# Optimization experiments

Measured on AMD Instinct MI355X. Metric: run time of the kernel, lower is better.

The kernel has to match this reference:

```python
import jax, jax.numpy as jnp
import numpy as np

E = 512      # embed_dim
H = 8        # num_heads
D = E // H   # head_dim = 64
R = 32       # rot_dims (partial rotary)
THETA = 10000.0


def _rope(x):
    # x: [B, H, S, D]; rotate first R dims (interleaved pairs, lucidrains-style)
    S = x.shape[-2]
    inv_freq = THETA ** (-jnp.arange(0, R, 2, dtype=jnp.float32) / R)  # [R/2]
    ang = jnp.arange(S, dtype=jnp.float32)[:, None] * inv_freq          # [S, R/2]
    c, s = jnp.cos(ang), jnp.sin(ang)
    xr, xp = x[..., :R], x[..., R:]
    x1, x2 = xr[..., 0::2], xr[..., 1::2]
    rot = jnp.stack([x1 * c - x2 * s, x1 * s + x2 * c], axis=-1).reshape(xr.shape)
    return jnp.concatenate([rot, xp], axis=-1)


def setup_inputs() -> dict:
    key = jax.random.key(0)
    k1, k2, k3, k4 = jax.random.split(key, 4)
    B, S = 4, 2048
    x = jax.random.normal(k1, (B, S, E), dtype=jnp.float32)
    input_mask = jax.random.randint(k2, (B, S), 0, 2).astype(bool)
    W_in = jax.random.normal(k3, (3 * E, E), dtype=jnp.float32) / np.sqrt(E).astype(np.float32)
    W_out = jax.random.normal(k4, (E, E), dtype=jnp.float32) / np.sqrt(E).astype(np.float32)
    return {"x": x, "input_mask": input_mask, "W_in": W_in, "W_out": W_out}


def reference(x, input_mask, W_in, W_out):
    B, S, _ = x.shape
    # fused QKV projection (Linear, no bias): x @ W_in.T -> [B,S,3E]
    qkv = (x @ W_in.T).reshape(B, S, 3, H, D).transpose(2, 0, 3, 1, 4)  # [3,B,H,S,D]
    q, k, v = qkv[0], qkv[1], qkv[2]
    q = _rope(q)
    k = _rope(k)
    # mask: causal AND (both tokens valid OR diagonal)
    causal = jnp.tril(jnp.ones((S, S), dtype=bool))
    inv = ~input_mask                                  # [B,S]
    cross = inv[:, None, :] | inv[:, :, None]          # [B,S,S]
    square = (~cross) | jnp.eye(S, dtype=bool)         # diagonal forced True
    full = causal[None, :, :] & square                 # [B,S,S]
    scores = jnp.einsum('bhsd,bhtd->bhst', q, k) / np.float32(np.sqrt(D))
    scores = jnp.where(full[:, None, :, :], scores, -jnp.inf)
    probs = jax.nn.softmax(scores, axis=-1)
    attn = jnp.einsum('bhst,bhtd->bhsd', probs, v)
    attn = attn.transpose(0, 2, 1, 3).reshape(B, S, E)
    return attn @ W_out.T
```

## Files before the change

kernel.cpp:

```cpp
#include <hip/hip_runtime.h>
#include <math.h>

#define B_ 4
#define S_ 2048
#define E_ 512
#define H_ 8
#define D_ 64

typedef short bf16x8 __attribute__((ext_vector_type(8)));
typedef float f32x4 __attribute__((ext_vector_type(4)));

__device__ inline short f2bf(float f) {
  union { float f; unsigned u; } v; v.f = f;
  unsigned r = v.u + 0x7FFF + ((v.u >> 16) & 1);
  return (short)(r >> 16);
}
__device__ inline short f2bf_fast(float f) {
  union { float f; unsigned u; } v; v.f = f;
  return (short)((v.u + 0x8000u) >> 16);
}
__device__ inline float bf2f(short s) {
  union { unsigned u; float f; } v; v.u = ((unsigned)(unsigned short)s) << 16;
  return v.f;
}

__global__ __launch_bounds__(256) void cvt_bf16(const float* __restrict__ src,
                                                short* __restrict__ dst, int n4) {
  int i = blockIdx.x * 256 + threadIdx.x;
  if (i < n4) {
    float4 f = ((const float4*)src)[i];
    short4 o;
    o.x = f2bf(f.x); o.y = f2bf(f.y); o.z = f2bf(f.z); o.w = f2bf(f.w);
    ((short4*)dst)[i] = o;
  }
}

__global__ __launch_bounds__(256) void gemm_qkv_mfma(
    const short* __restrict__ Xb,
    const short* __restrict__ Wb,
    short* __restrict__ qb, short* __restrict__ kb, short* __restrict__ vbT) {
  __shared__ __align__(16) short As[128][40];
  __shared__ __align__(16) short Bs[128][40];
  const int tid = threadIdx.x;
  const int w = tid >> 6, lane = tid & 63;
  const int l15 = lane & 15, quad = lane >> 4;
  const int wm = w & 1, wn = w >> 1;
  const int m0 = blockIdx.x * 128;
  const int n0 = blockIdx.y * 128;
  f32x4 acc[4][4];
  for (int mt = 0; mt < 4; ++mt)
    for (int nt = 0; nt < 4; ++nt) acc[mt][nt] = (f32x4){0.f, 0.f, 0.f, 0.f};

  for (int k0 = 0; k0 < E_; k0 += 32) {
    __syncthreads();
    for (int l = 0; l < 2; ++l) {
      int c = tid + 256 * l;
      int row = c >> 2, k8 = (c & 3) * 8;
      *(bf16x8*)&As[row][k8] = *(const bf16x8*)&Xb[(size_t)(m0 + row) * E_ + k0 + k8];
      *(bf16x8*)&Bs[row][k8] = *(const bf16x8*)&Wb[(size_t)(n0 + row) * E_ + k0 + k8];
    }
    __syncthreads();
    bf16x8 a[4], bfr[4];
    for (int mt = 0; mt < 4; ++mt)
      a[mt] = *(const bf16x8*)&As[wm * 64 + mt * 16 + l15][quad * 8];
    for (int nt = 0; nt < 4; ++nt)
      bfr[nt] = *(const bf16x8*)&Bs[wn * 64 + nt * 16 + l15][quad * 8];
    for (int mt = 0; mt < 4; ++mt)
      for (int nt = 0; nt < 4; ++nt)
        acc[mt][nt] = __builtin_amdgcn_mfma_f32_16x16x32_bf16(a[mt], bfr[nt], acc[mt][nt], 0, 0, 0);
  }
  const int t3 = n0 >> 9;
  for (int nt = 0; nt < 4; ++nt) {
    const int n = n0 + wn * 64 + nt * 16 + l15;
    const int h = (n >> 6) & 7;
    const int d = n & 63;
    const bool dorope = (t3 < 2) && (d < 32);
    const float sgn = (d & 1) ? 1.f : -1.f;
    const float fr = dorope ? powf(10000.f, -(float)(2 * (d >> 1)) * (1.f / 32.f)) : 0.f;
    for (int mt = 0; mt < 4; ++mt) {
      for (int i = 0; i < 4; ++i) {
        const int m = m0 + wm * 64 + mt * 16 + quad * 4 + i;
        const int b = m >> 11, s = m & (S_ - 1);
        float val = acc[mt][nt][i];
        float pv = __shfl_xor(val, 1, 64);
        float outv = val;
        if (dorope) {
          float ang = (float)s * fr;
          float sn, cs;
          sincosf(ang, &sn, &cs);
          outv = val * cs + pv * sgn * sn;
        }
        if (t3 == 2)
          vbT[((size_t)(b * 8 + h) * D_ + d) * S_ + s] = f2bf(outv);
        else {
          short* dst = (t3 == 0) ? qb : kb;
          dst[(((size_t)(b * 8 + h)) * S_ + s) * D_ + d] = f2bf(outv);
        }
      }
    }
  }
}

__global__ __launch_bounds__(256) void gemm_out_mfma(
    const short* __restrict__ Ab, const short* __restrict__ Wb,
    float* __restrict__ out) {
  __shared__ __align__(16) short As[128][40];
  __shared__ __align__(16) short Bs[128][40];
  const int tid = threadIdx.x;
  const int w = tid >> 6, lane = tid & 63;
  const int l15 = lane & 15, quad = lane >> 4;
  const int wm = w & 1, wn = w >> 1;
  const int m0 = blockIdx.x * 128;
  const int n0 = blockIdx.y * 128;
  f32x4 acc[4][4];
  for (int mt = 0; mt < 4; ++mt)
    for (int nt = 0; nt < 4; ++nt) acc[mt][nt] = (f32x4){0.f, 0.f, 0.f, 0.f};

  for (int k0 = 0; k0 < E_; k0 += 32) {
    __syncthreads();
    for (int l = 0; l < 2; ++l) {
      int c = tid + 256 * l;
      int row = c >> 2, k8 = (c & 3) * 8;
      *(bf16x8*)&As[row][k8] = *(const bf16x8*)&Ab[(size_t)(m0 + row) * E_ + k0 + k8];
      *(bf16x8*)&Bs[row][k8] = *(const bf16x8*)&Wb[(size_t)(n0 + row) * E_ + k0 + k8];
    }
    __syncthreads();
    bf16x8 a[4], bfr[4];
    for (int mt = 0; mt < 4; ++mt)
      a[mt] = *(const bf16x8*)&As[wm * 64 + mt * 16 + l15][quad * 8];
    for (int nt = 0; nt < 4; ++nt)
      bfr[nt] = *(const bf16x8*)&Bs[wn * 64 + nt * 16 + l15][quad * 8];
    for (int mt = 0; mt < 4; ++mt)
      for (int nt = 0; nt < 4; ++nt)
        acc[mt][nt] = __builtin_amdgcn_mfma_f32_16x16x32_bf16(a[mt], bfr[nt], acc[mt][nt], 0, 0, 0);
  }
  for (int mt = 0; mt < 4; ++mt)
    for (int nt = 0; nt < 4; ++nt) {
      const int n = n0 + wn * 64 + nt * 16 + l15;
      for (int i = 0; i < 4; ++i) {
        const int m = m0 + wm * 64 + mt * 16 + quad * 4 + i;
        out[(size_t)m * E_ + n] = acc[mt][nt][i];
      }
    }
}

__global__ __launch_bounds__(256) void flash_mfma(
    const short* __restrict__ qb, const short* __restrict__ kb,
    const short* __restrict__ vbT, const int* __restrict__ maskp,
    short* __restrict__ pb0, short* __restrict__ pb1,
    float* __restrict__ lb0, float* __restrict__ lb1,
    short* __restrict__ ob) {
  __shared__ __align__(16) short Ks[64][72];
  __shared__ __align__(16) short VT[64][72];
  __shared__ __align__(16) short Pl[4][16][72];
  __shared__ float kbias[64];
  const int tid = threadIdx.x;
  const int w = tid >> 6, lane = tid & 63;
  const int l15 = lane & 15, quad = lane >> 4;
  const int bid = blockIdx.x;
  const int u = bid & 7, v = bid >> 3;
  const int bh = (u << 2) | (v & 3);
  const int w2 = v >> 2;
  const int pair = w2 & 15;
  const int kh = w2 >> 4;
  const int b = bh >> 3, hd = bh & 7;
  const short* qbase = qb + (size_t)bh * S_ * D_;
  const short* kbase = kb + (size_t)bh * S_ * D_;
  const short* vtb   = vbT + (size_t)bh * D_ * S_;
  short* PB = kh ? pb1 : pb0;
  float* LB = kh ? lb1 : lb0;
  const float c2 = 0.1803368801f;
  bf16x8 ones;
  for (int j = 0; j < 8; ++j) ones[j] = (short)0x3F80;

  for (int seg = 0; seg < 2; ++seg) {
    const int qt = (seg == 0) ? pair : 31 - pair;
    const int r0 = qt * 64;
    const int mid = (qt + 2) >> 1;
    const int lo = kh ? mid : 0;
    const int hi = kh ? (qt + 1) : mid;
    bf16x8 aq[2];
    {
      const short* qrow = qbase + (size_t)(r0 + 16 * w + l15) * D_;
      aq[0] = *(const bf16x8*)&qrow[quad * 8];
      aq[1] = *(const bf16x8*)&qrow[32 + quad * 8];
    }
    f32x4 o[4], lsum;
    for (int no = 0; no < 4; ++no) o[no] = (f32x4){0.f, 0.f, 0.f, 0.f};
    lsum = (f32x4){0.f, 0.f, 0.f, 0.f};

    for (int kt = lo; kt < hi; ++kt) {
      const int t0 = kt * 64;
      __syncthreads();
      for (int l = 0; l < 2; ++l) {
        int idx = tid + 256 * l;
        int row = idx >> 3, ch = (idx & 7) * 8;
        *(bf16x8*)&Ks[row][ch] = *(const bf16x8*)(kbase + (size_t)(t0 + row) * D_ + ch);
        *(bf16x8*)&VT[row][ch] = *(const bf16x8*)(vtb + (size_t)row * S_ + t0 + ch);
      }
      if (tid < 64)
        kbias[tid] = maskp[b * S_ + t0 + tid] ? -23.08312f : -1.0e38f;
      __syncthreads();
      f32x4 sfr[4];
      for (int nb = 0; nb < 4; ++nb) sfr[nb] = (f32x4){0.f, 0.f, 0.f, 0.f};
      for (int nb = 0; nb < 4; ++nb)
        for (int ks = 0; ks < 2; ++ks) {
          bf16x8 bk = *(const bf16x8*)&Ks[l15 + 16 * nb][32 * ks + quad * 8];
          sfr[nb] = __builtin_amdgcn_mfma_f32_16x16x32_bf16(aq[ks], bk, sfr[nb], 0, 0, 0);
        }
      if (kt < qt) {
        for (int nb = 0; nb < 4; ++nb) {
          const float bb = kbias[l15 + 16 * nb];
          for (int i = 0; i < 4; ++i)
            Pl[w][quad * 4 + i][l15 + 16 * nb] = f2bf_fast(exp2f(sfr[nb][i] * c2 + bb));
        }
      } else {
        for (int nb = 0; nb < 4; ++nb) {
          const int tg = l15 + 16 * nb;
          const float bb = kbias[l15 + 16 * nb];
          for (int i = 0; i < 4; ++i) {
            const float bbi = (tg > 16 * w + quad * 4 + i) ? -1.0e38f : bb;
            Pl[w][quad * 4 + i][l15 + 16 * nb] = f2bf_fast(exp2f(sfr[nb][i] * c2 + bbi));
          }
        }
      }
      asm volatile("s_waitcnt lgkmcnt(0)" ::: "memory");
      bf16x8 ap0 = *(const bf16x8*)&Pl[w][l15][quad * 8];
      bf16x8 ap1 = *(const bf16x8*)&Pl[w][l15][32 + quad * 8];
      for (int no = 0; no < 4; ++no) {
        bf16x8 bv0 = *(const bf16x8*)&VT[16 * no + l15][quad * 8];
        bf16x8 bv1 = *(const bf16x8*)&VT[16 * no + l15][32 + quad * 8];
        o[no] = __builtin_amdgcn_mfma_f32_16x16x32_bf16(ap0, bv0, o[no], 0, 0, 0);
        o[no] = __builtin_amdgcn_mfma_f32_16x16x32_bf16(ap1, bv1, o[no], 0, 0, 0);
      }
      lsum = __builtin_amdgcn_mfma_f32_16x16x32_bf16(ap0, ones, lsum, 0, 0, 0);
      lsum = __builtin_amdgcn_mfma_f32_16x16x32_bf16(ap1, ones, lsum, 0, 0, 0);
    }
    for (int i = 0; i < 4; ++i) {
      const int s = r0 + 16 * w + quad * 4 + i;
      const int qm = maskp[b * S_ + s];
      const size_t row = (size_t)(b * S_ + s) * E_ + hd * D_;
      if (kh == 0 && !qm) {
        for (int no = 0; no < 4; ++no) {
          const int d = l15 + 16 * no;
          ob[row + d] = vtb[(size_t)d * S_ + s];
        }
      }
      for (int no = 0; no < 4; ++no)
        PB[row + l15 + 16 * no] = f2bf(o[no][i]);
      if (l15 == 0)
        LB[bh * S_ + s] = lsum[i];
    }
  }
}

__global__ __launch_bounds__(256) void merge_kernel(
    const short* __restrict__ pb0, const short* __restrict__ pb1,
    const float* __restrict__ lb0, const float* __restrict__ lb1,
    const int* __restrict__ maskp, short* __restrict__ ob) {
  int idx = blockIdx.x * 256 + threadIdx.x;
  int m = idx >> 6, e = (idx & 63) * 8;
  if (!maskp[m]) return;
  int b = m >> 11, s = m & (S_ - 1);
  int bh = b * 8 + (e >> 6);
  float l = lb0[bh * S_ + s] + lb1[bh * S_ + s];
  float inv = 1.f / l;
  bf16x8 p0 = *(const bf16x8*)&pb0[(size_t)m * E_ + e];
  bf16x8 p1 = *(const bf16x8*)&pb1[(size_t)m * E_ + e];
  bf16x8 r;
  for (int j = 0; j < 8; ++j)
    r[j] = f2bf((bf2f(p0[j]) + bf2f(p1[j])) * inv);
  *(bf16x8*)&ob[(size_t)m * E_ + e] = r;
}

extern "C" void kernel_launch(void* const* d_in, const int* in_sizes, int n_in,
                              void* d_out, int out_size, void* d_ws, size_t ws_size,
                              hipStream_t stream) {
  const float* x    = (const float*)d_in[0];
  const int*   mask = (const int*)d_in[1];
  const float* Win  = (const float*)d_in[2];
  const float* Wout = (const float*)d_in[3];
  float* out = (float*)d_out;

  short* Xb    = (short*)d_ws;
  short* Winb  = Xb + 8192 * 512;
  short* Woutb = Winb + 1536 * 512;
  short* qb    = Woutb + 512 * 512;
  short* kb    = qb + 32 * 2048 * 64;
  short* vbT   = kb + 32 * 2048 * 64;
  short* ob    = vbT + 32 * 2048 * 64;
  short* pb0   = ob + 8192 * 512;
  short* pb1   = pb0 + 8192 * 512;
  float* lb0   = (float*)(pb1 + 8192 * 512);
  float* lb1   = lb0 + 32 * 2048;

  cvt_bf16<<<4096, 256, 0, stream>>>(x, Xb, 8192 * 512 / 4);
  cvt_bf16<<<768, 256, 0, stream>>>(Win, Winb, 1536 * 512 / 4);
  cvt_bf16<<<256, 256, 0, stream>>>(Wout, Woutb, 512 * 512 / 4);
  gemm_qkv_mfma<<<dim3(64, 12), 256, 0, stream>>>(Xb, Winb, qb, kb, vbT);
  flash_mfma<<<1024, 256, 0, stream>>>(qb, kb, vbT, mask, pb0, pb1, lb0, lb1, ob);
  merge_kernel<<<2048, 256, 0, stream>>>(pb0, pb1, lb0, lb1, mask, ob);
  gemm_out_mfma<<<dim3(64, 4), 256, 0, stream>>>(ob, Woutb, out);
}
```

Before: 178.3 us.

## Double-buffer LDS in projection GEMMs and merge conversion launches

Both projection GEMMs now use two LDS buffers: the global loads for the next K-slice are issued into registers before the MFMAs on the current slice and stored to the other buffer afterwards, leaving one barrier per iteration instead of two. The three fp32-to-bf16 conversion kernels are merged into one launch that picks its source by block index. The RoPE epilogue switches sincosf to the faster, lower-precision __sincosf intrinsic. The aim is to hide global load latency and cut launch overhead, at the cost of doubled LDS use and more live registers.

```diff
diff --git a/kernel.cpp b/kernel.cpp
--- a/kernel.cpp
+++ b/kernel.cpp
@@ -24,50 +24,78 @@
   return v.f;
 }
 
-__global__ __launch_bounds__(256) void cvt_bf16(const float* __restrict__ src,
-                                                short* __restrict__ dst, int n4) {
-  int i = blockIdx.x * 256 + threadIdx.x;
-  if (i < n4) {
-    float4 f = ((const float4*)src)[i];
-    short4 o;
-    o.x = f2bf(f.x); o.y = f2bf(f.y); o.z = f2bf(f.z); o.w = f2bf(f.w);
-    ((short4*)dst)[i] = o;
-  }
+__global__ __launch_bounds__(256) void cvt_all(
+    const float* __restrict__ x, const float* __restrict__ win,
+    const float* __restrict__ wout, short* __restrict__ xb,
+    short* __restrict__ winb, short* __restrict__ woutb) {
+  int bid = blockIdx.x;
+  const float* src; short* dst; int i;
+  if (bid < 4096)      { src = x;    dst = xb;    i = bid * 256 + threadIdx.x; }
+  else if (bid < 4864) { src = win;  dst = winb;  i = (bid - 4096) * 256 + threadIdx.x; }
+  else                 { src = wout; dst = woutb; i = (bid - 4864) * 256 + threadIdx.x; }
+  float4 f = ((const float4*)src)[i];
+  short4 o;
+  o.x = f2bf(f.x); o.y = f2bf(f.y); o.z = f2bf(f.z); o.w = f2bf(f.w);
+  ((short4*)dst)[i] = o;
 }
 
 __global__ __launch_bounds__(256) void gemm_qkv_mfma(
     const short* __restrict__ Xb,
     const short* __restrict__ Wb,
     short* __restrict__ qb, short* __restrict__ kb, short* __restrict__ vbT) {
-  __shared__ __align__(16) short As[128][40];
-  __shared__ __align__(16) short Bs[128][40];
+  __shared__ __align__(16) short As[2][128][40];
+  __shared__ __align__(16) short Bs[2][128][40];
   const int tid = threadIdx.x;
   const int w = tid >> 6, lane = tid & 63;
   const int l15 = lane & 15, quad = lane >> 4;
   const int wm = w & 1, wn = w >> 1;
   const int m0 = blockIdx.x * 128;
   const int n0 = blockIdx.y * 128;
+  const int r0s = tid >> 2,        k80 = (tid & 3) * 8;
+  const int r1s = (tid + 256) >> 2, k81 = ((tid + 256) & 3) * 8;
+  const short* gA0 = &Xb[(size_t)(m0 + r0s) * E_ + k80];
+  const short* gA1 = &Xb[(size_t)(m0 + r1s) * E_ + k81];
+  const short* gB0 = &Wb[(size_t)(n0 + r0s) * E_ + k80];
+  const short* gB1 = &Wb[(size_t)(n0 + r1s) * E_ + k81];
   f32x4 acc[4][4];
   for (int mt = 0; mt < 4; ++mt)
     for (int nt = 0; nt < 4; ++nt) acc[mt][nt] = (f32x4){0.f, 0.f, 0.f, 0.f};
 
-  for (int k0 = 0; k0 < E_; k0 += 32) {
-    __syncthreads();
-    for (int l = 0; l < 2; ++l) {
-      int c = tid + 256 * l;
-      int row = c >> 2, k8 = (c & 3) * 8;
-      *(bf16x8*)&As[row][k8] = *(const bf16x8*)&Xb[(size_t)(m0 + row) * E_ + k0 + k8];
-      *(bf16x8*)&Bs[row][k8] = *(const bf16x8*)&Wb[(size_t)(n0 + row) * E_ + k0 + k8];
-    }
-    __syncthreads();
+  bf16x8 ra0 = *(const bf16x8*)gA0;
+  bf16x8 ra1 = *(const bf16x8*)gA1;
+  bf16x8 rb0 = *(const bf16x8*)gB0;
+  bf16x8 rb1 = *(const bf16x8*)gB1;
+  *(bf16x8*)&As[0][r0s][k80] = ra0;
+  *(bf16x8*)&As[0][r1s][k81] = ra1;
+  *(bf16x8*)&Bs[0][r0s][k80] = rb0;
+  *(bf16x8*)&Bs[0][r1s][k81] = rb1;
+  __syncthreads();
+
+  for (int kt = 0; kt < 16; ++kt) {
+    const int cur = kt & 1;
+    if (kt < 15) {
+      const int k0 = (kt + 1) * 32;
+      ra0 = *(const bf16x8*)(gA0 + k0);
+      ra1 = *(const bf16x8*)(gA1 + k0);
+      rb0 = *(const bf16x8*)(gB0 + k0);
+      rb1 = *(const bf16x8*)(gB1 + k0);
+    }
     bf16x8 a[4], bfr[4];
     for (int mt = 0; mt < 4; ++mt)
-      a[mt] = *(const bf16x8*)&As[wm * 64 + mt * 16 + l15][quad * 8];
+      a[mt] = *(const bf16x8*)&As[cur][wm * 64 + mt * 16 + l15][quad * 8];
     for (int nt = 0; nt < 4; ++nt)
-      bfr[nt] = *(const bf16x8*)&Bs[wn * 64 + nt * 16 + l15][quad * 8];
+      bfr[nt] = *(const bf16x8*)&Bs[cur][wn * 64 + nt * 16 + l15][quad * 8];
     for (int mt = 0; mt < 4; ++mt)
       for (int nt = 0; nt < 4; ++nt)
         acc[mt][nt] = __builtin_amdgcn_mfma_f32_16x16x32_bf16(a[mt], bfr[nt], acc[mt][nt], 0, 0, 0);
+    if (kt < 15) {
+      const int nxt = cur ^ 1;
+      *(bf16x8*)&As[nxt][r0s][k80] = ra0;
+      *(bf16x8*)&As[nxt][r1s][k81] = ra1;
+      *(bf16x8*)&Bs[nxt][r0s][k80] = rb0;
+      *(bf16x8*)&Bs[nxt][r1s][k81] = rb1;
+    }
+    __syncthreads();
   }
   const int t3 = n0 >> 9;
   for (int nt = 0; nt < 4; ++nt) {
@@ -85,9 +113,8 @@
         float pv = __shfl_xor(val, 1, 64);
         float outv = val;
         if (dorope) {
-          float ang = (float)s * fr;
           float sn, cs;
-          sincosf(ang, &sn, &cs);
+          __sincosf((float)s * fr, &sn, &cs);
           outv = val * cs + pv * sgn * sn;
         }
         if (t3 == 2)
@@ -104,35 +131,59 @@
 __global__ __launch_bounds__(256) void gemm_out_mfma(
     const short* __restrict__ Ab, const short* __restrict__ Wb,
     float* __restrict__ out) {
-  __shared__ __align__(16) short As[128][40];
-  __shared__ __align__(16) short Bs[128][40];
+  __shared__ __align__(16) short As[2][128][40];
+  __shared__ __align__(16) short Bs[2][128][40];
   const int tid = threadIdx.x;
   const int w = tid >> 6, lane = tid & 63;
   const int l15 = lane & 15, quad = lane >> 4;
   const int wm = w & 1, wn = w >> 1;
   const int m0 = blockIdx.x * 128;
   const int n0 = blockIdx.y * 128;
+  const int r0s = tid >> 2,        k80 = (tid & 3) * 8;
+  const int r1s = (tid + 256) >> 2, k81 = ((tid + 256) & 3) * 8;
+  const short* gA0 = &Ab[(size_t)(m0 + r0s) * E_ + k80];
+  const short* gA1 = &Ab[(size_t)(m0 + r1s) * E_ + k81];
+  const short* gB0 = &Wb[(size_t)(n0 + r0s) * E_ + k80];
+  const short* gB1 = &Wb[(size_t)(n0 + r1s) * E_ + k81];
   f32x4 acc[4][4];
   for (int mt = 0; mt < 4; ++mt)
     for (int nt = 0; nt < 4; ++nt) acc[mt][nt] = (f32x4){0.f, 0.f, 0.f, 0.f};
 
-  for (int k0 = 0; k0 < E_; k0 += 32) {
-    __syncthreads();
-    for (int l = 0; l < 2; ++l) {
-      int c = tid + 256 * l;
-      int row = c >> 2, k8 = (c & 3) * 8;
-      *(bf16x8*)&As[row][k8] = *(const bf16x8*)&Ab[(size_t)(m0 + row) * E_ + k0 + k8];
-      *(bf16x8*)&Bs[row][k8] = *(const bf16x8*)&Wb[(size_t)(n0 + row) * E_ + k0 + k8];
-    }
-    __syncthreads();
+  bf16x8 ra0 = *(const bf16x8*)gA0;
+  bf16x8 ra1 = *(const bf16x8*)gA1;
+  bf16x8 rb0 = *(const bf16x8*)gB0;
+  bf16x8 rb1 = *(const bf16x8*)gB1;
+  *(bf16x8*)&As[0][r0s][k80] = ra0;
+  *(bf16x8*)&As[0][r1s][k81] = ra1;
+  *(bf16x8*)&Bs[0][r0s][k80] = rb0;
+  *(bf16x8*)&Bs[0][r1s][k81] = rb1;
+  __syncthreads();
+
+  for (int kt = 0; kt < 16; ++kt) {
+    const int cur = kt & 1;
+    if (kt < 15) {
+      const int k0 = (kt + 1) * 32;
+      ra0 = *(const bf16x8*)(gA0 + k0);
+      ra1 = *(const bf16x8*)(gA1 + k0);
+      rb0 = *(const bf16x8*)(gB0 + k0);
+      rb1 = *(const bf16x8*)(gB1 + k0);
+    }
     bf16x8 a[4], bfr[4];
     for (int mt = 0; mt < 4; ++mt)
-      a[mt] = *(const bf16x8*)&As[wm * 64 + mt * 16 + l15][quad * 8];
+      a[mt] = *(const bf16x8*)&As[cur][wm * 64 + mt * 16 + l15][quad * 8];
     for (int nt = 0; nt < 4; ++nt)
-      bfr[nt] = *(const bf16x8*)&Bs[wn * 64 + nt * 16 + l15][quad * 8];
+      bfr[nt] = *(const bf16x8*)&Bs[cur][wn * 64 + nt * 16 + l15][quad * 8];
     for (int mt = 0; mt < 4; ++mt)
       for (int nt = 0; nt < 4; ++nt)
         acc[mt][nt] = __builtin_amdgcn_mfma_f32_16x16x32_bf16(a[mt], bfr[nt], acc[mt][nt], 0, 0, 0);
+    if (kt < 15) {
+      const int nxt = cur ^ 1;
+      *(bf16x8*)&As[nxt][r0s][k80] = ra0;
+      *(bf16x8*)&As[nxt][r1s][k81] = ra1;
+      *(bf16x8*)&Bs[nxt][r0s][k80] = rb0;
+      *(bf16x8*)&Bs[nxt][r1s][k81] = rb1;
+    }
+    __syncthreads();
   }
   for (int mt = 0; mt < 4; ++mt)
     for (int nt = 0; nt < 4; ++nt) {
@@ -294,9 +345,7 @@
   float* lb0   = (float*)(pb1 + 8192 * 512);
   float* lb1   = lb0 + 32 * 2048;
 
-  cvt_bf16<<<4096, 256, 0, stream>>>(x, Xb, 8192 * 512 / 4);
-  cvt_bf16<<<768, 256, 0, stream>>>(Win, Winb, 1536 * 512 / 4);
-  cvt_bf16<<<256, 256, 0, stream>>>(Wout, Woutb, 512 * 512 / 4);
+  cvt_all<<<5120, 256, 0, stream>>>(x, Win, Wout, Xb, Winb, Woutb);
   gemm_qkv_mfma<<<dim3(64, 12), 256, 0, stream>>>(Xb, Winb, qb, kb, vbT);
   flash_mfma<<<1024, 256, 0, stream>>>(qb, kb, vbT, mask, pb0, pb1, lb0, lb1, ob);
   merge_kernel<<<2048, 256, 0, stream>>>(pb0, pb1, lb0, lb1, mask, ob);
```

Measured after the change: 265.7 us. 1.49x slower.
